# Performance work log

Hardware: AMD Instinct MI355X
Metric: run time of the kernel (lower is better)

## Reference

```python
import jax, jax.numpy as jnp
import numpy as np

N = 20000      # nodes (human PPI network scale)
E = 640000     # edges (avg degree 32)
PE, GOS, PROT = 128, 128, 480
OM_DIMS = [3, 3, 24, 24]          # transcriptome, proteome, effectome, interactome
D = 384                           # latent_space_dimension = 128 * 3 (jk 'cat')
H = 128                           # hidden_channels per layer
NEG_SLOPE = 0.1


def setup_inputs() -> dict:
    key = jax.random.key(0)
    ks = jax.random.split(key, 64)
    rn = lambda k, shp, s=0.05: jax.random.normal(k, shp, jnp.float32) * s
    inp = {
        "x": jax.random.normal(ks[0], (N, PE + GOS + PROT), jnp.float32),
        "x_ft": jax.random.normal(ks[1], (N, sum(OM_DIMS)), jnp.float32),
        "edge_index": jax.random.randint(ks[2], (2, E), 0, N),
    }
    i = 3
    def lin(fin, fout, name):
        nonlocal i
        inp["W_" + name] = rn(ks[i], (fin, fout)); inp["b_" + name] = jnp.zeros((fout,), jnp.float32)
        i += 1
    lin(PE, D, "pe"); lin(GOS, D, "gos"); lin(PROT, D, "prot")
    for j, d in enumerate(OM_DIMS):
        lin(d, D, f"om{j}")
    dims = [D, H, H, H]
    for j in range(3):
        lin(dims[j], dims[j + 1], f"c{j}")   # feature-branch GCN convs
        lin(dims[j], dims[j + 1], f"o{j}")   # omics-branch GCN convs
    lin(2 * D, D, "lat")
    lin(D, H, "drug"); lin(D, H, "dis")
    lin(H, 2, "odrug"); lin(H, 2, "odis")
    return inp


def _gcn(x, W, b, src, dst, deg_inv):
    # GCNConv(improved=True): A_hat = A + 2I, sym norm D^-1/2 A_hat D^-1/2
    h = x @ W                                  # [N, F_out]
    coef = deg_inv[src] * deg_inv[dst]         # [E]
    agg = jax.ops.segment_sum(h[src] * coef[:, None], dst, num_segments=N)
    agg = agg + h * (2.0 * deg_inv * deg_inv)[:, None]   # self loops (weight 2)
    return agg + b


def reference(x, x_ft, edge_index,
              W_pe, b_pe, W_gos, b_gos, W_prot, b_prot,
              W_om0, b_om0, W_om1, b_om1, W_om2, b_om2, W_om3, b_om3,
              W_c0, b_c0, W_o0, b_o0, W_c1, b_c1, W_o1, b_o1, W_c2, b_c2, W_o2, b_o2,
              W_lat, b_lat, W_drug, b_drug, W_dis, b_dis,
              W_odrug, b_odrug, W_odis, b_odis):
    act = lambda t: jax.nn.leaky_relu(t, NEG_SLOPE)
    src, dst = edge_index[0], edge_index[1]
    deg = jax.ops.segment_sum(jnp.ones((E,), jnp.float32), dst, num_segments=N) + 2.0
    deg_inv = jax.lax.rsqrt(deg)

    # encoders (features branch): pe | gosemsim | prot_emb slices of x
    pe = x[:, :PE]; gos = x[:, PE:PE + GOS]; prot = x[:, PE + GOS:PE + GOS + PROT]
    h = act(pe @ W_pe + b_pe + gos @ W_gos + b_gos + prot @ W_prot + b_prot)

    # encoders (omics branch): 3|3|24|24 slices of x_ft
    offs = np.cumsum([0] + OM_DIMS)
    Wom = [W_om0, W_om1, W_om2, W_om3]; bom = [b_om0, b_om1, b_om2, b_om3]
    g = act(sum(x_ft[:, offs[j]:offs[j + 1]] @ Wom[j] + bom[j] for j in range(4)))

    Wc = [W_c0, W_c1, W_c2]; bc = [b_c0, b_c1, b_c2]
    Wo = [W_o0, W_o1, W_o2]; bo = [b_o0, b_o1, b_o2]
    hs, gs = [], []
    for j in range(3):
        h = act(_gcn(h, Wc[j], bc[j], src, dst, deg_inv)); hs.append(h)
        g = act(_gcn(g, Wo[j], bo[j], src, dst, deg_inv)); gs.append(g)
    jk = jnp.concatenate(hs, axis=-1)          # [N, 384]
    jk_om = jnp.concatenate(gs, axis=-1)       # [N, 384]

    z = act(jnp.concatenate([jk, jk_om], axis=-1) @ W_lat + b_lat)  # [N, 384]
    drug = act(z @ W_drug + b_drug) @ W_odrug + b_odrug             # [N, 2]
    dis = act(z @ W_dis + b_dis) @ W_odis + b_odis                  # [N, 2]
    return jnp.concatenate([drug, dis], axis=-1)                    # [N, 4]
```

## Files before the change

kernel.cpp:

```cpp
#include <hip/hip_runtime.h>
#include <cstdint>

#define NN 20000
#define NNP 20096
#define NE 640000
#define NEG_SLOPE 0.1f
#define NSCAN 79
#define NSL 8
#define NPSL 2500
#define FBPS 160
#define NPART 8

typedef unsigned short ushort_t;
typedef __attribute__((ext_vector_type(8))) short short8;
typedef __attribute__((ext_vector_type(4))) float f32x4;
typedef __attribute__((ext_vector_type(2))) float f32x2;

__device__ __forceinline__ unsigned short f2bf(float f) {
    union { float f; unsigned u; } v; v.f = f;
    unsigned r = v.u + 0x7fffu + ((v.u >> 16) & 1u);
    return (unsigned short)(r >> 16);
}
__device__ __forceinline__ float bflo(unsigned u) { return __uint_as_float(u << 16); }
__device__ __forceinline__ float bfhi(unsigned u) { return __uint_as_float(u & 0xffff0000u); }

__device__ __forceinline__ int swz(int r) { return (r ^ (r >> 2)) & 3; }

__device__ __forceinline__ void gld_lds16(const void* g, void* l) {
    __builtin_amdgcn_global_load_lds(
        (const __attribute__((address_space(1))) void*)g,
        (__attribute__((address_space(3))) void*)l,
        16, 0, 0);
}

#define O_CAT   0
#define O_OM    282624
#define O_C0    307200
#define O_O0    356352
#define O_C1    405504
#define O_O1    421888
#define O_C2    438272
#define O_O2    454656
#define O_LAT   471040
#define O_HEADS 765952
#define WT_TOTAL 864256

__global__ __launch_bounds__(256) void pack_weights(
    const float* __restrict__ Wpe, const float* __restrict__ Wgos, const float* __restrict__ Wprot,
    const float* __restrict__ bpe, const float* __restrict__ bgos, const float* __restrict__ bprot,
    const float* __restrict__ Wom0, const float* __restrict__ Wom1,
    const float* __restrict__ Wom2, const float* __restrict__ Wom3,
    const float* __restrict__ bom0, const float* __restrict__ bom1,
    const float* __restrict__ bom2, const float* __restrict__ bom3,
    const float* __restrict__ Wc0, const float* __restrict__ Wo0,
    const float* __restrict__ Wc1, const float* __restrict__ Wo1,
    const float* __restrict__ Wc2, const float* __restrict__ Wo2,
    const float* __restrict__ Wlat,
    const float* __restrict__ Wdrug, const float* __restrict__ Wdis,
    const float* __restrict__ bdrug, const float* __restrict__ bdis,
    ushort_t* __restrict__ Wt, float* __restrict__ bcat, float* __restrict__ bomc,
    float* __restrict__ bheads, int* __restrict__ cnt8)
{
    int i = blockIdx.x * blockDim.x + threadIdx.x;
    if (i < 282624) {
        int m = i / 736, k = i % 736;
        float v = (k < 128) ? Wpe[k * 384 + m]
                : (k < 256) ? Wgos[(k - 128) * 384 + m]
                            : Wprot[(k - 256) * 384 + m];
        Wt[O_CAT + i] = f2bf(v);
        return;
    }
    i -= 282624;
    if (i < 24576) {
        int m = i / 64, k = i % 64;
        float v = (k < 3)  ? Wom0[k * 384 + m]
                : (k < 6)  ? Wom1[(k - 3) * 384 + m]
                : (k < 30) ? Wom2[(k - 6) * 384 + m]
                : (k < 54) ? Wom3[(k - 30) * 384 + m] : 0.f;
        Wt[O_OM + i] = f2bf(v);
        return;
    }
    i -= 24576;
    if (i < 49152) { int m = i / 384, k = i % 384; Wt[O_C0 + i] = f2bf(Wc0[k * 128 + m]); return; }
    i -= 49152;
    if (i < 49152) { int m = i / 384, k = i % 384; Wt[O_O0 + i] = f2bf(Wo0[k * 128 + m]); return; }
    i -= 49152;
    if (i < 16384) { int m = i / 128, k = i % 128; Wt[O_C1 + i] = f2bf(Wc1[k * 128 + m]); return; }
    i -= 16384;
    if (i < 16384) { int m = i / 128, k = i % 128; Wt[O_O1 + i] = f2bf(Wo1[k * 128 + m]); return; }
    i -= 16384;
    if (i < 16384) { int m = i / 128, k = i % 128; Wt[O_C2 + i] = f2bf(Wc2[k * 128 + m]); return; }
    i -= 16384;
    if (i < 16384) { int m = i / 128, k = i % 128; Wt[O_O2 + i] = f2bf(Wo2[k * 128 + m]); return; }
    i -= 16384;
    if (i < 294912) { int m = i / 768, k = i % 768; Wt[O_LAT + i] = f2bf(Wlat[k * 384 + m]); return; }
    i -= 294912;
    if (i < 98304) {
        int m = i / 384, k = i % 384;
        float v = (m < 128) ? Wdrug[k * 128 + m] : Wdis[k * 128 + (m - 128)];
        Wt[O_HEADS + i] = f2bf(v);
        return;
    }
    i -= 98304;
    if (i < 384) { bcat[i] = bpe[i] + bgos[i] + bprot[i]; return; }
    i -= 384;
    if (i < 384) { bomc[i] = bom0[i] + bom1[i] + bom2[i] + bom3[i]; return; }
    i -= 384;
    if (i < 256) { bheads[i] = (i < 128) ? bdrug[i] : bdis[i - 128]; return; }
    i -= 256;
    if (i < NN * NPART) { cnt8[i] = 0; return; }
}
#define PACK_TOTAL (WT_TOTAL + 384 + 384 + 256 + NN * NPART)

#define CVT_T1 (NN * 736 / 4)
__global__ __launch_bounds__(256) void convert_inputs(
    const float* __restrict__ x, const float* __restrict__ xft,
    ushort_t* __restrict__ xb, ushort_t* __restrict__ xftb)
{
    int i = blockIdx.x * blockDim.x + threadIdx.x;
    if (i < CVT_T1) {
        int base = i * 4;
        float4 v = *reinterpret_cast<const float4*>(&x[base]);
        unsigned long long p = (unsigned long long)f2bf(v.x)
                             | ((unsigned long long)f2bf(v.y) << 16)
                             | ((unsigned long long)f2bf(v.z) << 32)
                             | ((unsigned long long)f2bf(v.w) << 48);
        *reinterpret_cast<unsigned long long*>(&xb[base]) = p;
        return;
    }
    i -= CVT_T1;
    if (i < NN * 64) {
        int r = i >> 6, c = i & 63;
        float v = (c < 54) ? xft[r * 54 + c] : 0.f;
        xftb[i] = f2bf(v);
    }
}

__global__ __launch_bounds__(256) void count_deg_sliced(
    const int* __restrict__ src, const int* __restrict__ dst, int* __restrict__ cnt8)
{
    const int slice = blockIdx.x & (NSL - 1);
    const int blk = blockIdx.x >> 3;
    const int lo = slice * NPSL, hi = lo + NPSL;
    for (int e = blk * 256 + threadIdx.x; e < NE; e += FBPS * 256) {
        int d = dst[e];
        if (d >= lo && d < hi) {
            int p = (unsigned)src[e] / 2500u;
            atomicAdd(&cnt8[d * NPART + p], 1);
        }
    }
}

__global__ __launch_bounds__(256) void scan_blocksums(const int* __restrict__ cnt8, int* __restrict__ bsum,
                                                      float* __restrict__ deg_inv)
{
    __shared__ int s[256];
    int t = threadIdx.x, i = blockIdx.x * 256 + t;
    int v = 0;
    if (i < NN) {
        uint4 a = *reinterpret_cast<const uint4*>(&cnt8[i * NPART]);
        uint4 b = *reinterpret_cast<const uint4*>(&cnt8[i * NPART + 4]);
        v = (int)(a.x + a.y + a.z + a.w + b.x + b.y + b.z + b.w);
        deg_inv[i] = rsqrtf((float)v + 2.0f);
    }
    s[t] = v;
    __syncthreads();
    for (int off = 128; off; off >>= 1) {
        if (t < off) s[t] += s[t + off];
        __syncthreads();
    }
    if (t == 0) bsum[blockIdx.x] = s[0];
}

__global__ __launch_bounds__(128) void scan_tops(const int* __restrict__ bsum,
                                                 int* __restrict__ boff, int* __restrict__ ofsN)
{
    __shared__ int s[NSCAN];
    int t = threadIdx.x;
    if (t < NSCAN) s[t] = bsum[t];
    __syncthreads();
    if (t == 0) {
        int run = 0;
        for (int b = 0; b < NSCAN; b++) { int x = s[b]; s[b] = run; run += x; }
        ofsN[NN] = run;
    }
    __syncthreads();
    if (t < NSCAN) boff[t] = s[t];
}

__global__ __launch_bounds__(256) void scan_apply(const int* __restrict__ cnt8, const int* __restrict__ boff,
                                                  int* __restrict__ ofsN, int* __restrict__ cursor8)
{
    __shared__ int s[256];
    int t = threadIdx.x, i = blockIdx.x * 256 + t;
    int c[NPART];
    int v = 0;
    if (i < NN) {
        uint4 a = *reinterpret_cast<const uint4*>(&cnt8[i * NPART]);
        uint4 b = *reinterpret_cast<const uint4*>(&cnt8[i * NPART + 4]);
        c[0] = a.x; c[1] = a.y; c[2] = a.z; c[3] = a.w;
        c[4] = b.x; c[5] = b.y; c[6] = b.z; c[7] = b.w;
#pragma unroll
        for (int p = 0; p < NPART; p++) v += c[p];
    }
    s[t] = v;
    __syncthreads();
    for (int off = 1; off < 256; off <<= 1) {
        int u = (t >= off) ? s[t - off] : 0;
        __syncthreads();
        s[t] += u;
        __syncthreads();
    }
    if (i < NN) {
        int run = s[t] - v + boff[blockIdx.x];
        ofsN[i] = run;
#pragma unroll
        for (int p = 0; p < NPART; p++) { cursor8[i * NPART + p] = run; run += c[p]; }
    }
}

__global__ __launch_bounds__(256) void fill_csr_sliced(
    const int* __restrict__ src, const int* __restrict__ dst,
    const float* __restrict__ deg_inv, int* __restrict__ cursor8,
    uint2* __restrict__ csr_pk)
{
    const int slice = blockIdx.x & (NSL - 1);
    const int blk = blockIdx.x >> 3;
    const int lo = slice * NPSL, hi = lo + NPSL;
    for (int e = blk * 256 + threadIdx.x; e < NE; e += FBPS * 256) {
        int d = dst[e];
        if (d >= lo && d < hi) {
            int s = src[e];
            int pp = (unsigned)s / 2500u;
            int p = atomicAdd(&cursor8[d * NPART + pp], 1);
            float cf = deg_inv[s] * deg_inv[d];
            csr_pk[p] = make_uint2((unsigned)s * 512u, __float_as_uint(cf));
        }
    }
}

template<int BN, bool BIASACT, bool OUT_BF16>
__device__ __forceinline__ void gemm_body(
    ushort_t* As, ushort_t* Bs,
    const ushort_t* __restrict__ A, int lda,
    const ushort_t* __restrict__ Wt,
    const float* __restrict__ bias,
    float* __restrict__ Cf, ushort_t* __restrict__ Cb, int ldc,
    int nrows, int K, int row0, int col0)
{
    constexpr int BK = 32;
    constexpr int NI = (BN == 128) ? 4 : 2;

    const int t = threadIdx.x;
    const int w = t >> 6, lane = t & 63;
    const int wr = w >> 1, wc = w & 1;
    const int m16 = lane & 15, quad = lane >> 4;
    const int sr = lane >> 2;
    const int pgrp = lane & 3;

    f32x4 acc[4][NI];
#pragma unroll
    for (int mi = 0; mi < 4; mi++)
#pragma unroll
        for (int ni = 0; ni < NI; ni++) acc[mi][ni] = (f32x4)0.f;

    for (int k0 = 0; k0 < K; k0 += BK) {
#pragma unroll
        for (int p = 0; p < 2; p++) {
            int c = p * 4 + w;
            int r = c * 16 + sr;
            int q = pgrp ^ swz(r);
            gld_lds16(&A[(size_t)(row0 + r) * lda + k0 + q * 8], &As[c * 512]);
        }
#pragma unroll
        for (int p = 0; p < BN / 64; p++) {
            int c = p * 4 + w;
            int r = c * 16 + sr;
            int q = pgrp ^ swz(r);
            gld_lds16(&Wt[(size_t)(col0 + r) * K + k0 + q * 8], &Bs[c * 512]);
        }
        __syncthreads();

        short8 af[4], bfr[NI];
#pragma unroll
        for (int mi = 0; mi < 4; mi++) {
            int r = wr * 64 + mi * 16 + m16;
            int p = quad ^ swz(r);
            af[mi] = *reinterpret_cast<const short8*>(&As[r * 32 + p * 8]);
        }
#pragma unroll
        for (int ni = 0; ni < NI; ni++) {
            int n = wc * (NI * 16) + ni * 16 + m16;
            int p = quad ^ swz(n);
            bfr[ni] = *reinterpret_cast<const short8*>(&Bs[n * 32 + p * 8]);
        }
#pragma unroll
        for (int mi = 0; mi < 4; mi++)
#pragma unroll
            for (int ni = 0; ni < NI; ni++)
                acc[mi][ni] = __builtin_amdgcn_mfma_f32_16x16x32_bf16(af[mi], bfr[ni], acc[mi][ni], 0, 0, 0);
        __syncthreads();
    }

#pragma unroll
    for (int mi = 0; mi < 4; mi++) {
#pragma unroll
        for (int reg = 0; reg < 4; reg++) {
            int grow = row0 + wr * 64 + mi * 16 + quad * 4 + reg;
            if (grow >= nrows) continue;
#pragma unroll
            for (int ni = 0; ni < NI; ni++) {
                int gcol = col0 + wc * (NI * 16) + ni * 16 + m16;
                float v = acc[mi][ni][reg];
                if constexpr (BIASACT) {
                    v += bias[gcol];
                    v = (v > 0.f) ? v : NEG_SLOPE * v;
                }
                if constexpr (OUT_BF16) Cb[(size_t)grow * ldc + gcol] = f2bf(v);
                else                    Cf[(size_t)grow * ldc + gcol] = v;
            }
        }
    }
}

template<int BN, bool BIASACT, bool OUT_BF16>
__global__ __launch_bounds__(256) void mfma_gemm(
    const ushort_t* __restrict__ A, int lda,
    const ushort_t* __restrict__ Wt,
    const float* __restrict__ bias,
    float* __restrict__ Cf, ushort_t* __restrict__ Cb, int ldc,
    int nrows, int K)
{
    __shared__ ushort_t As[128 * 32];
    __shared__ ushort_t Bs[BN * 32];
    gemm_body<BN, BIASACT, OUT_BF16>(As, Bs, A, lda, Wt, bias, Cf, Cb, ldc, nrows, K,
                                     blockIdx.y * 128, blockIdx.x * BN);
}

__global__ __launch_bounds__(256) void mfma_gemm_dual(
    const ushort_t* __restrict__ A0, const ushort_t* __restrict__ A1, int lda,
    const ushort_t* __restrict__ W0, const ushort_t* __restrict__ W1,
    ushort_t* __restrict__ tmpI,
    int nrows, int K)
{
    __shared__ ushort_t As[128 * 32];
    __shared__ ushort_t Bs[64 * 32];
    const ushort_t* A  = blockIdx.z ? A1 : A0;
    const ushort_t* Wt = blockIdx.z ? W1 : W0;
    ushort_t*       Cb = tmpI + blockIdx.z * 128;
    gemm_body<64, false, true>(As, Bs, A, lda, Wt, nullptr, nullptr, Cb, 256, nrows, K,
                               blockIdx.y * 128, blockIdx.x * 64);
}

__global__ __launch_bounds__(256) void aggregate_fused(
    const ushort_t* __restrict__ tabI,
    const float* __restrict__ bc, const float* __restrict__ bo,
    const int* __restrict__ ofsN, const uint2* __restrict__ csr_pk,
    const float* __restrict__ deg_inv,
    ushort_t* __restrict__ outb, int hcol, int gcol)
{
    const int w = threadIdx.x >> 6, lane = threadIdx.x & 63;
    const int i = blockIdx.x * 4 + w;
    const int el = lane >> 5;
    const int fq = lane & 31;
    const int chain = fq >> 4;
    const unsigned lbyte = (unsigned)(fq * 16);
    const char* __restrict__ tb = (const char*)tabI;

    const int start = ofsN[i], end = ofsN[i + 1];
    const float di = deg_inv[i];
    const uint4 pv = *reinterpret_cast<const uint4*>(tb + ((unsigned)i * 512u + lbyte));

    float acc[8];
#pragma unroll
    for (int q = 0; q < 8; q++) acc[q] = 0.f;

#define FMA8(P, C) \
    acc[0] = fmaf(bflo(P.x), C, acc[0]); acc[1] = fmaf(bfhi(P.x), C, acc[1]); \
    acc[2] = fmaf(bflo(P.y), C, acc[2]); acc[3] = fmaf(bfhi(P.y), C, acc[3]); \
    acc[4] = fmaf(bflo(P.z), C, acc[4]); acc[5] = fmaf(bfhi(P.z), C, acc[5]); \
    acc[6] = fmaf(bflo(P.w), C, acc[6]); acc[7] = fmaf(bfhi(P.w), C, acc[7])

    int j = start + el;
    for (; j + 6 < end; j += 8) {
        uint2 e0 = csr_pk[j];
        uint2 e1 = csr_pk[j + 2];
        uint2 e2 = csr_pk[j + 4];
        uint2 e3 = csr_pk[j + 6];
        uint4 p0 = *reinterpret_cast<const uint4*>(tb + (e0.x + lbyte));
        uint4 p1 = *reinterpret_cast<const uint4*>(tb + (e1.x + lbyte));
        uint4 p2 = *reinterpret_cast<const uint4*>(tb + (e2.x + lbyte));
        uint4 p3 = *reinterpret_cast<const uint4*>(tb + (e3.x + lbyte));
        float c0 = __uint_as_float(e0.y), c1 = __uint_as_float(e1.y);
        float c2 = __uint_as_float(e2.y), c3 = __uint_as_float(e3.y);
        FMA8(p0, c0); FMA8(p1, c1); FMA8(p2, c2); FMA8(p3, c3);
    }
    for (; j < end; j += 2) {
        uint2 e0 = csr_pk[j];
        uint4 p0 = *reinterpret_cast<const uint4*>(tb + (e0.x + lbyte));
        float c0 = __uint_as_float(e0.y);
        FMA8(p0, c0);
    }
#undef FMA8

#pragma unroll
    for (int q = 0; q < 8; q++) acc[q] += __shfl_xor(acc[q], 32);

    if (el == 0) {
        const float* __restrict__ bias = chain ? bo : bc;
        const int coloff = (fq & 15) * 8;
        const float c = 2.f * di * di;
        float sv[8] = {bflo(pv.x), bfhi(pv.x), bflo(pv.y), bfhi(pv.y),
                       bflo(pv.z), bfhi(pv.z), bflo(pv.w), bfhi(pv.w)};
        uint4 o;
        unsigned* op = &o.x;
#pragma unroll
        for (int q = 0; q < 8; q += 2) {
            float v0 = fmaf(sv[q],     c, acc[q])     + bias[coloff + q];
            float v1 = fmaf(sv[q + 1], c, acc[q + 1]) + bias[coloff + q + 1];
            v0 = (v0 > 0.f) ? v0 : NEG_SLOPE * v0;
            v1 = (v1 > 0.f) ? v1 : NEG_SLOPE * v1;
            op[q >> 1] = (unsigned)f2bf(v0) | ((unsigned)f2bf(v1) << 16);
        }
        const int col = (chain ? gcol : hcol) + coloff;
        *reinterpret_cast<uint4*>(&outb[(size_t)i * 768 + col]) = o;
    }
}

__global__ __launch_bounds__(256) void heads_kernel(
    const float* __restrict__ tmpH,
    const float* __restrict__ Wod, const float* __restrict__ bod,
    const float* __restrict__ Wos, const float* __restrict__ bos,
    float* __restrict__ out)
{
    int w = threadIdx.x >> 6, lane = threadIdx.x & 63;
    int i = blockIdx.x * 4 + w;
    if (i >= NN) return;
    float a0 = 0.f, a1 = 0.f, d0 = 0.f, d1 = 0.f;
#pragma unroll
    for (int p = 0; p < 2; p++) {
        int k = lane + p * 64;
        float vd = tmpH[(size_t)i * 256 + k];
        float vs = tmpH[(size_t)i * 256 + 128 + k];
        a0 = fmaf(vd, Wod[k * 2 + 0], a0);
        a1 = fmaf(vd, Wod[k * 2 + 1], a1);
        d0 = fmaf(vs, Wos[k * 2 + 0], d0);
        d1 = fmaf(vs, Wos[k * 2 + 1], d1);
    }
    for (int off = 32; off; off >>= 1) {
        a0 += __shfl_down(a0, off);
        a1 += __shfl_down(a1, off);
        d0 += __shfl_down(d0, off);
        d1 += __shfl_down(d1, off);
    }
    if (lane == 0) {
        out[(size_t)i * 4 + 0] = a0 + bod[0];
        out[(size_t)i * 4 + 1] = a1 + bod[1];
        out[(size_t)i * 4 + 2] = d0 + bos[0];
        out[(size_t)i * 4 + 3] = d1 + bos[1];
    }
}

extern "C" void kernel_launch(void* const* d_in, const int* in_sizes, int n_in,
                              void* d_out, int out_size, void* d_ws, size_t ws_size,
                              hipStream_t stream)
{
    const float* x      = (const float*)d_in[0];
    const float* x_ft   = (const float*)d_in[1];
    const int*   eidx   = (const int*)d_in[2];
    const float* W_pe   = (const float*)d_in[3];
    const float* b_pe   = (const float*)d_in[4];
    const float* W_gos  = (const float*)d_in[5];
    const float* b_gos  = (const float*)d_in[6];
    const float* W_prot = (const float*)d_in[7];
    const float* b_prot = (const float*)d_in[8];
    const float* W_om0  = (const float*)d_in[9];
    const float* b_om0  = (const float*)d_in[10];
    const float* W_om1  = (const float*)d_in[11];
    const float* b_om1  = (const float*)d_in[12];
    const float* W_om2  = (const float*)d_in[13];
    const float* b_om2  = (const float*)d_in[14];
    const float* W_om3  = (const float*)d_in[15];
    const float* b_om3  = (const float*)d_in[16];
    const float* W_c[3] = {(const float*)d_in[17], (const float*)d_in[21], (const float*)d_in[25]};
    const float* b_c[3] = {(const float*)d_in[18], (const float*)d_in[22], (const float*)d_in[26]};
    const float* W_o[3] = {(const float*)d_in[19], (const float*)d_in[23], (const float*)d_in[27]};
    const float* b_o[3] = {(const float*)d_in[20], (const float*)d_in[24], (const float*)d_in[28]};
    const float* W_lat  = (const float*)d_in[29];
    const float* b_lat  = (const float*)d_in[30];
    const float* W_drug = (const float*)d_in[31];
    const float* b_drug = (const float*)d_in[32];
    const float* W_dis  = (const float*)d_in[33];
    const float* b_dis  = (const float*)d_in[34];
    const float* W_odrug= (const float*)d_in[35];
    const float* b_odrug= (const float*)d_in[36];
    const float* W_odis = (const float*)d_in[37];
    const float* b_odis = (const float*)d_in[38];
    float* out = (float*)d_out;

    const int* e_src = eidx;
    const int* e_dst = eidx + NE;

    char* p = (char*)d_ws;
    auto alloc = [&](size_t bytes) -> void* {
        void* r = (void*)p;
        p += (bytes + 255) & ~(size_t)255;
        return r;
    };
    ushort_t* Wt    = (ushort_t*)alloc((size_t)WT_TOTAL * 2);
    float* bcat     = (float*)alloc(384 * 4);
    float* bomc     = (float*)alloc(384 * 4);
    float* bheads   = (float*)alloc(256 * 4);
    float* deg_inv  = (float*)alloc((size_t)NN * 4);
    int*   cnt8     = (int*)alloc((size_t)NN * NPART * 4);
    int*   cursor8  = (int*)alloc((size_t)NN * NPART * 4);
    int*   ofsN     = (int*)alloc((size_t)(NN + 1) * 4);
    int*   bsum     = (int*)alloc((size_t)NSCAN * 4);
    int*   boff     = (int*)alloc((size_t)NSCAN * 4);
    uint2* csr_pk   = (uint2*)alloc((size_t)NE * 8);
    ushort_t* xb    = (ushort_t*)alloc((size_t)NNP * 736 * 2);
    ushort_t* xftb  = (ushort_t*)alloc((size_t)NNP * 64 * 2);
    ushort_t* h0b   = (ushort_t*)alloc((size_t)NNP * 384 * 2);
    ushort_t* g0b   = (ushort_t*)alloc((size_t)NNP * 384 * 2);
    ushort_t* jkb   = (ushort_t*)alloc((size_t)NNP * 768 * 2);
    ushort_t* zb    = (ushort_t*)alloc((size_t)NNP * 384 * 2);
    ushort_t* tmpI  = (ushort_t*)alloc((size_t)NNP * 256 * 2);
    float* tmpH     = (float*)alloc((size_t)NNP * 256 * 4);
    (void)ws_size; (void)in_sizes; (void)n_in; (void)out_size;

    pack_weights<<<dim3((PACK_TOTAL + 255) / 256), dim3(256), 0, stream>>>(
        W_pe, W_gos, W_prot, b_pe, b_gos, b_prot,
        W_om0, W_om1, W_om2, W_om3, b_om0, b_om1, b_om2, b_om3,
        W_c[0], W_o[0], W_c[1], W_o[1], W_c[2], W_o[2],
        W_lat, W_drug, W_dis, b_drug, b_dis, Wt, bcat, bomc, bheads, cnt8);

    convert_inputs<<<dim3((CVT_T1 + NN * 64 + 255) / 256), dim3(256), 0, stream>>>(x, x_ft, xb, xftb);

    count_deg_sliced<<<dim3(NSL * FBPS), dim3(256), 0, stream>>>(e_src, e_dst, cnt8);
    scan_blocksums<<<dim3(NSCAN), dim3(256), 0, stream>>>(cnt8, bsum, deg_inv);
    scan_tops<<<dim3(1), dim3(128), 0, stream>>>(bsum, boff, ofsN);
    scan_apply<<<dim3(NSCAN), dim3(256), 0, stream>>>(cnt8, boff, ofsN, cursor8);
    fill_csr_sliced<<<dim3(NSL * FBPS), dim3(256), 0, stream>>>(e_src, e_dst, deg_inv, cursor8, csr_pk);

    mfma_gemm<128, true, true><<<dim3(3, 157), dim3(256), 0, stream>>>(
        xb, 736, Wt + O_CAT, bcat, nullptr, h0b, 384, NN, 736);
    mfma_gemm<128, true, true><<<dim3(3, 157), dim3(256), 0, stream>>>(
        xftb, 64, Wt + O_OM, bomc, nullptr, g0b, 384, NN, 64);

    mfma_gemm_dual<<<dim3(2, 157, 2), dim3(256), 0, stream>>>(
        h0b, g0b, 384, Wt + O_C0, Wt + O_O0, tmpI, NN, 384);
    aggregate_fused<<<dim3(NN / 4), dim3(256), 0, stream>>>(
        tmpI, b_c[0], b_o[0], ofsN, csr_pk, deg_inv, jkb, 0, 384);

    mfma_gemm_dual<<<dim3(2, 157, 2), dim3(256), 0, stream>>>(
        jkb + 0, jkb + 384, 768, Wt + O_C1, Wt + O_O1, tmpI, NN, 128);
    aggregate_fused<<<dim3(NN / 4), dim3(256), 0, stream>>>(
        tmpI, b_c[1], b_o[1], ofsN, csr_pk, deg_inv, jkb, 128, 512);

    mfma_gemm_dual<<<dim3(2, 157, 2), dim3(256), 0, stream>>>(
        jkb + 128, jkb + 512, 768, Wt + O_C2, Wt + O_O2, tmpI, NN, 128);
    aggregate_fused<<<dim3(NN / 4), dim3(256), 0, stream>>>(
        tmpI, b_c[2], b_o[2], ofsN, csr_pk, deg_inv, jkb, 256, 640);

    mfma_gemm<128, true, true><<<dim3(3, 157), dim3(256), 0, stream>>>(
        jkb, 768, Wt + O_LAT, b_lat, nullptr, zb, 384, NN, 768);

    mfma_gemm<128, true, false><<<dim3(2, 157), dim3(256), 0, stream>>>(
        zb, 384, Wt + O_HEADS, bheads, tmpH, nullptr, 256, NN, 384);
    heads_kernel<<<dim3((NN + 3) / 4), dim3(256), 0, stream>>>(
        tmpH, W_odrug, b_odrug, W_odis, b_odis, out);
}
```

Baseline: 480.1 us.

## Merge prologue kernels, fuse scan tops, merge encoder GEMMs, fuse output heads

Weight packing, input conversion and degree counting now run in one launch, with cnt8 zeroed by a memset. The single-block scan_tops kernel is folded into scan_apply, where every block redundantly computes the block offsets. The two encoder GEMMs share one launch via blockIdx.z. The heads GEMM now applies bias, leaky-relu and the 2-wide output projection in its epilogue, so the fp32 intermediate tmpH and heads_kernel are gone. The aim is fewer launches and less global traffic, at the cost of more complex epilogues and the degree counting sharing a launch with conversion work.

```diff
diff --git a/kernel.cpp b/kernel.cpp
--- a/kernel.cpp
+++ b/kernel.cpp
@@ -14,7 +14,6 @@
 typedef unsigned short ushort_t;
 typedef __attribute__((ext_vector_type(8))) short short8;
 typedef __attribute__((ext_vector_type(4))) float f32x4;
-typedef __attribute__((ext_vector_type(2))) float f32x2;
 
 __device__ __forceinline__ unsigned short f2bf(float f) {
     union { float f; unsigned u; } v; v.f = f;
@@ -45,7 +44,16 @@
 #define O_HEADS 765952
 #define WT_TOTAL 864256
 
-__global__ __launch_bounds__(256) void pack_weights(
+#define PACK_TOTAL (WT_TOTAL + 384 + 384 + 256)
+#define CVT_T1 (NN * 736 / 4)
+#define P1_CNTB (NSL * FBPS)
+#define P1_CVTB ((CVT_T1 + NN * 64 + 255) / 256)
+#define P1_PKB  (PACK_TOTAL / 256)
+
+__global__ __launch_bounds__(256) void phase1(
+    const int* __restrict__ esrc, const int* __restrict__ edst, int* __restrict__ cnt8,
+    const float* __restrict__ x, const float* __restrict__ xft,
+    ushort_t* __restrict__ xb, ushort_t* __restrict__ xftb,
     const float* __restrict__ Wpe, const float* __restrict__ Wgos, const float* __restrict__ Wprot,
     const float* __restrict__ bpe, const float* __restrict__ bgos, const float* __restrict__ bprot,
     const float* __restrict__ Wom0, const float* __restrict__ Wom1,
@@ -59,95 +67,91 @@
     const float* __restrict__ Wdrug, const float* __restrict__ Wdis,
     const float* __restrict__ bdrug, const float* __restrict__ bdis,
     ushort_t* __restrict__ Wt, float* __restrict__ bcat, float* __restrict__ bomc,
-    float* __restrict__ bheads, int* __restrict__ cnt8)
-{
-    int i = blockIdx.x * blockDim.x + threadIdx.x;
-    if (i < 282624) {
-        int m = i / 736, k = i % 736;
-        float v = (k < 128) ? Wpe[k * 384 + m]
-                : (k < 256) ? Wgos[(k - 128) * 384 + m]
-                            : Wprot[(k - 256) * 384 + m];
-        Wt[O_CAT + i] = f2bf(v);
+    float* __restrict__ bheads)
+{
+    int bx = blockIdx.x;
+    if (bx < P1_CNTB) {
+        const int slice = bx & (NSL - 1);
+        const int blk = bx >> 3;
+        const int lo = slice * NPSL, hi = lo + NPSL;
+        for (int e = blk * 256 + threadIdx.x; e < NE; e += FBPS * 256) {
+            int d = edst[e];
+            if (d >= lo && d < hi) {
+                int p = (unsigned)esrc[e] / 2500u;
+                atomicAdd(&cnt8[d * NPART + p], 1);
+            }
+        }
         return;
     }
-    i -= 282624;
-    if (i < 24576) {
-        int m = i / 64, k = i % 64;
-        float v = (k < 3)  ? Wom0[k * 384 + m]
-                : (k < 6)  ? Wom1[(k - 3) * 384 + m]
-                : (k < 30) ? Wom2[(k - 6) * 384 + m]
-                : (k < 54) ? Wom3[(k - 30) * 384 + m] : 0.f;
-        Wt[O_OM + i] = f2bf(v);
+    bx -= P1_CNTB;
+    if (bx < P1_CVTB) {
+        int i = bx * 256 + threadIdx.x;
+        if (i < CVT_T1) {
+            int base = i * 4;
+            float4 v = *reinterpret_cast<const float4*>(&x[base]);
+            unsigned long long p = (unsigned long long)f2bf(v.x)
+                                 | ((unsigned long long)f2bf(v.y) << 16)
+                                 | ((unsigned long long)f2bf(v.z) << 32)
+                                 | ((unsigned long long)f2bf(v.w) << 48);
+            *reinterpret_cast<unsigned long long*>(&xb[base]) = p;
+            return;
+        }
+        i -= CVT_T1;
+        if (i < NN * 64) {
+            int r = i >> 6, c = i & 63;
+            float v = (c < 54) ? xft[r * 54 + c] : 0.f;
+            xftb[i] = f2bf(v);
+        }
         return;
     }
-    i -= 24576;
-    if (i < 49152) { int m = i / 384, k = i % 384; Wt[O_C0 + i] = f2bf(Wc0[k * 128 + m]); return; }
-    i -= 49152;
-    if (i < 49152) { int m = i / 384, k = i % 384; Wt[O_O0 + i] = f2bf(Wo0[k * 128 + m]); return; }
-    i -= 49152;
-    if (i < 16384) { int m = i / 128, k = i % 128; Wt[O_C1 + i] = f2bf(Wc1[k * 128 + m]); return; }
-    i -= 16384;
-    if (i < 16384) { int m = i / 128, k = i % 128; Wt[O_O1 + i] = f2bf(Wo1[k * 128 + m]); return; }
-    i -= 16384;
-    if (i < 16384) { int m = i / 128, k = i % 128; Wt[O_C2 + i] = f2bf(Wc2[k * 128 + m]); return; }
-    i -= 16384;
-    if (i < 16384) { int m = i / 128, k = i % 128; Wt[O_O2 + i] = f2bf(Wo2[k * 128 + m]); return; }
-    i -= 16384;
-    if (i < 294912) { int m = i / 768, k = i % 768; Wt[O_LAT + i] = f2bf(Wlat[k * 384 + m]); return; }
-    i -= 294912;
-    if (i < 98304) {
-        int m = i / 384, k = i % 384;
-        float v = (m < 128) ? Wdrug[k * 128 + m] : Wdis[k * 128 + (m - 128)];
-        Wt[O_HEADS + i] = f2bf(v);
-        return;
-    }
-    i -= 98304;
-    if (i < 384) { bcat[i] = bpe[i] + bgos[i] + bprot[i]; return; }
-    i -= 384;
-    if (i < 384) { bomc[i] = bom0[i] + bom1[i] + bom2[i] + bom3[i]; return; }
-    i -= 384;
-    if (i < 256) { bheads[i] = (i < 128) ? bdrug[i] : bdis[i - 128]; return; }
-    i -= 256;
-    if (i < NN * NPART) { cnt8[i] = 0; return; }
-}
-#define PACK_TOTAL (WT_TOTAL + 384 + 384 + 256 + NN * NPART)
-
-#define CVT_T1 (NN * 736 / 4)
-__global__ __launch_bounds__(256) void convert_inputs(
-    const float* __restrict__ x, const float* __restrict__ xft,
-    ushort_t* __restrict__ xb, ushort_t* __restrict__ xftb)
-{
-    int i = blockIdx.x * blockDim.x + threadIdx.x;
-    if (i < CVT_T1) {
-        int base = i * 4;
-        float4 v = *reinterpret_cast<const float4*>(&x[base]);
-        unsigned long long p = (unsigned long long)f2bf(v.x)
-                             | ((unsigned long long)f2bf(v.y) << 16)
-                             | ((unsigned long long)f2bf(v.z) << 32)
-                             | ((unsigned long long)f2bf(v.w) << 48);
-        *reinterpret_cast<unsigned long long*>(&xb[base]) = p;
-        return;
-    }
-    i -= CVT_T1;
-    if (i < NN * 64) {
-        int r = i >> 6, c = i & 63;
-        float v = (c < 54) ? xft[r * 54 + c] : 0.f;
-        xftb[i] = f2bf(v);
-    }
-}
-
-__global__ __launch_bounds__(256) void count_deg_sliced(
-    const int* __restrict__ src, const int* __restrict__ dst, int* __restrict__ cnt8)
-{
-    const int slice = blockIdx.x & (NSL - 1);
-    const int blk = blockIdx.x >> 3;
-    const int lo = slice * NPSL, hi = lo + NPSL;
-    for (int e = blk * 256 + threadIdx.x; e < NE; e += FBPS * 256) {
-        int d = dst[e];
-        if (d >= lo && d < hi) {
-            int p = (unsigned)src[e] / 2500u;
-            atomicAdd(&cnt8[d * NPART + p], 1);
-        }
+    bx -= P1_CVTB;
+    {
+        int i = bx * 256 + threadIdx.x;
+        if (i < 282624) {
+            int m = i / 736, k = i % 736;
+            float v = (k < 128) ? Wpe[k * 384 + m]
+                    : (k < 256) ? Wgos[(k - 128) * 384 + m]
+                                : Wprot[(k - 256) * 384 + m];
+            Wt[O_CAT + i] = f2bf(v);
+            return;
+        }
+        i -= 282624;
+        if (i < 24576) {
+            int m = i / 64, k = i % 64;
+            float v = (k < 3)  ? Wom0[k * 384 + m]
+                    : (k < 6)  ? Wom1[(k - 3) * 384 + m]
+                    : (k < 30) ? Wom2[(k - 6) * 384 + m]
+                    : (k < 54) ? Wom3[(k - 30) * 384 + m] : 0.f;
+            Wt[O_OM + i] = f2bf(v);
+            return;
+        }
+        i -= 24576;
+        if (i < 49152) { int m = i / 384, k = i % 384; Wt[O_C0 + i] = f2bf(Wc0[k * 128 + m]); return; }
+        i -= 49152;
+        if (i < 49152) { int m = i / 384, k = i % 384; Wt[O_O0 + i] = f2bf(Wo0[k * 128 + m]); return; }
+        i -= 49152;
+        if (i < 16384) { int m = i / 128, k = i % 128; Wt[O_C1 + i] = f2bf(Wc1[k * 128 + m]); return; }
+        i -= 16384;
+        if (i < 16384) { int m = i / 128, k = i % 128; Wt[O_O1 + i] = f2bf(Wo1[k * 128 + m]); return; }
+        i -= 16384;
+        if (i < 16384) { int m = i / 128, k = i % 128; Wt[O_C2 + i] = f2bf(Wc2[k * 128 + m]); return; }
+        i -= 16384;
+        if (i < 16384) { int m = i / 128, k = i % 128; Wt[O_O2 + i] = f2bf(Wo2[k * 128 + m]); return; }
+        i -= 16384;
+        if (i < 294912) { int m = i / 768, k = i % 768; Wt[O_LAT + i] = f2bf(Wlat[k * 384 + m]); return; }
+        i -= 294912;
+        if (i < 98304) {
+            int m = i / 384, k = i % 384;
+            float v = (m < 128) ? Wdrug[k * 128 + m] : Wdis[k * 128 + (m - 128)];
+            Wt[O_HEADS + i] = f2bf(v);
+            return;
+        }
+        i -= 98304;
+        if (i < 384) { bcat[i] = bpe[i] + bgos[i] + bprot[i]; return; }
+        i -= 384;
+        if (i < 384) { bomc[i] = bom0[i] + bom1[i] + bom2[i] + bom3[i]; return; }
+        i -= 384;
+        if (i < 256) { bheads[i] = (i < 128) ? bdrug[i] : bdis[i - 128]; return; }
     }
 }
 
@@ -172,27 +176,22 @@
     if (t == 0) bsum[blockIdx.x] = s[0];
 }
 
-__global__ __launch_bounds__(128) void scan_tops(const int* __restrict__ bsum,
-                                                 int* __restrict__ boff, int* __restrict__ ofsN)
-{
-    __shared__ int s[NSCAN];
-    int t = threadIdx.x;
-    if (t < NSCAN) s[t] = bsum[t];
+__global__ __launch_bounds__(256) void scan_apply(const int* __restrict__ cnt8, const int* __restrict__ bsum,
+                                                  int* __restrict__ ofsN, int* __restrict__ cursor8)
+{
+    __shared__ int s[256];
+    __shared__ int sb[NSCAN];
+    int t = threadIdx.x, i = blockIdx.x * 256 + t;
+    if (t < NSCAN) sb[t] = bsum[t];
     __syncthreads();
     if (t == 0) {
         int run = 0;
-        for (int b = 0; b < NSCAN; b++) { int x = s[b]; s[b] = run; run += x; }
-        ofsN[NN] = run;
+        for (int b = 0; b < NSCAN; b++) { int x2 = sb[b]; sb[b] = run; run += x2; }
+        if (blockIdx.x == 0) ofsN[NN] = run;
     }
     __syncthreads();
-    if (t < NSCAN) boff[t] = s[t];
-}
-
-__global__ __launch_bounds__(256) void scan_apply(const int* __restrict__ cnt8, const int* __restrict__ boff,
-                                                  int* __restrict__ ofsN, int* __restrict__ cursor8)
-{
-    __shared__ int s[256];
-    int t = threadIdx.x, i = blockIdx.x * 256 + t;
+    const int boff = sb[blockIdx.x];
+
     int c[NPART];
     int v = 0;
     if (i < NN) {
@@ -212,7 +211,7 @@
         __syncthreads();
     }
     if (i < NN) {
-        int run = s[t] - v + boff[blockIdx.x];
+        int run = s[t] - v + boff;
         ofsN[i] = run;
 #pragma unroll
         for (int p = 0; p < NPART; p++) { cursor8[i * NPART + p] = run; run += c[p]; }
@@ -239,14 +238,12 @@
     }
 }
 
-template<int BN, bool BIASACT, bool OUT_BF16>
-__device__ __forceinline__ void gemm_body(
+template<int BN>
+__device__ __forceinline__ void gemm_core(
     ushort_t* As, ushort_t* Bs,
     const ushort_t* __restrict__ A, int lda,
-    const ushort_t* __restrict__ Wt,
-    const float* __restrict__ bias,
-    float* __restrict__ Cf, ushort_t* __restrict__ Cb, int ldc,
-    int nrows, int K, int row0, int col0)
+    const ushort_t* __restrict__ Wt, int K, int row0, int col0,
+    f32x4 (&acc)[4][(BN == 128) ? 4 : 2])
 {
     constexpr int BK = 32;
     constexpr int NI = (BN == 128) ? 4 : 2;
@@ -258,7 +255,6 @@
     const int sr = lane >> 2;
     const int pgrp = lane & 3;
 
-    f32x4 acc[4][NI];
 #pragma unroll
     for (int mi = 0; mi < 4; mi++)
 #pragma unroll
@@ -301,7 +297,20 @@
                 acc[mi][ni] = __builtin_amdgcn_mfma_f32_16x16x32_bf16(af[mi], bfr[ni], acc[mi][ni], 0, 0, 0);
         __syncthreads();
     }
-
+}
+
+template<int BN, bool BIASACT, bool OUT_BF16>
+__device__ __forceinline__ void gemm_store(
+    const f32x4 (&acc)[4][(BN == 128) ? 4 : 2],
+    const float* __restrict__ bias,
+    float* __restrict__ Cf, ushort_t* __restrict__ Cb, int ldc,
+    int nrows, int row0, int col0)
+{
+    constexpr int NI = (BN == 128) ? 4 : 2;
+    const int t = threadIdx.x;
+    const int w = t >> 6, lane = t & 63;
+    const int wr = w >> 1, wc = w & 1;
+    const int m16 = lane & 15, quad = lane >> 4;
 #pragma unroll
     for (int mi = 0; mi < 4; mi++) {
 #pragma unroll
@@ -333,8 +342,29 @@
 {
     __shared__ ushort_t As[128 * 32];
     __shared__ ushort_t Bs[BN * 32];
-    gemm_body<BN, BIASACT, OUT_BF16>(As, Bs, A, lda, Wt, bias, Cf, Cb, ldc, nrows, K,
-                                     blockIdx.y * 128, blockIdx.x * BN);
+    f32x4 acc[4][(BN == 128) ? 4 : 2];
+    gemm_core<BN>(As, Bs, A, lda, Wt, K, blockIdx.y * 128, blockIdx.x * BN, acc);
+    gemm_store<BN, BIASACT, OUT_BF16>(acc, bias, Cf, Cb, ldc, nrows,
+                                      blockIdx.y * 128, blockIdx.x * BN);
+}
+
+__global__ __launch_bounds__(256) void mfma_gemm_mlp(
+    const ushort_t* __restrict__ xb, const ushort_t* __restrict__ xftb,
+    const ushort_t* __restrict__ Wt,
+    const float* __restrict__ bcat, const float* __restrict__ bomc,
+    ushort_t* __restrict__ h0b, ushort_t* __restrict__ g0b)
+{
+    __shared__ ushort_t As[128 * 32];
+    __shared__ ushort_t Bs[128 * 32];
+    f32x4 acc[4][4];
+    const int row0 = blockIdx.y * 128, col0 = blockIdx.x * 128;
+    if (blockIdx.z == 0) {
+        gemm_core<128>(As, Bs, xb, 736, Wt + O_CAT, 736, row0, col0, acc);
+        gemm_store<128, true, true>(acc, bcat, nullptr, h0b, 384, NN, row0, col0);
+    } else {
+        gemm_core<128>(As, Bs, xftb, 64, Wt + O_OM, 64, row0, col0, acc);
+        gemm_store<128, true, true>(acc, bomc, nullptr, g0b, 384, NN, row0, col0);
+    }
 }
 
 __global__ __launch_bounds__(256) void mfma_gemm_dual(
@@ -348,8 +378,90 @@
     const ushort_t* A  = blockIdx.z ? A1 : A0;
     const ushort_t* Wt = blockIdx.z ? W1 : W0;
     ushort_t*       Cb = tmpI + blockIdx.z * 128;
-    gemm_body<64, false, true>(As, Bs, A, lda, Wt, nullptr, nullptr, Cb, 256, nrows, K,
-                               blockIdx.y * 128, blockIdx.x * 64);
+    f32x4 acc[4][2];
+    gemm_core<64>(As, Bs, A, lda, Wt, K, blockIdx.y * 128, blockIdx.x * 64, acc);
+    gemm_store<64, false, true>(acc, nullptr, nullptr, Cb, 256, nrows,
+                                blockIdx.y * 128, blockIdx.x * 64);
+}
+
+__global__ __launch_bounds__(256) void mfma_gemm_heads(
+    const ushort_t* __restrict__ zb, const ushort_t* __restrict__ Wt,
+    const float* __restrict__ bheads,
+    const float* __restrict__ Wod, const float* __restrict__ bod,
+    const float* __restrict__ Wos, const float* __restrict__ bos,
+    float* __restrict__ out)
+{
+    __shared__ ushort_t As[128 * 32];
+    __shared__ ushort_t Bs[128 * 32];
+    f32x4 acc[4][4];
+    const int row0 = blockIdx.y * 128, col0 = blockIdx.x * 128;
+    gemm_core<128>(As, Bs, zb, 384, Wt + O_HEADS, 384, row0, col0, acc);
+
+    const float* __restrict__ Wh = col0 ? Wos : Wod;
+    const float* __restrict__ bh = col0 ? bos : bod;
+    const int t = threadIdx.x;
+    const int w = t >> 6, lane = t & 63;
+    const int wr = w >> 1, wc = w & 1;
+    const int m16 = lane & 15, quad = lane >> 4;
+
+    float w0[4], w1[4];
+#pragma unroll
+    for (int ni = 0; ni < 4; ni++) {
+        int k = wc * 64 + ni * 16 + m16;
+        w0[ni] = Wh[k * 2 + 0];
+        w1[ni] = Wh[k * 2 + 1];
+    }
+    float p0[16], p1[16];
+#pragma unroll
+    for (int mi = 0; mi < 4; mi++) {
+#pragma unroll
+        for (int reg = 0; reg < 4; reg++) {
+            float s0 = 0.f, s1 = 0.f;
+#pragma unroll
+            for (int ni = 0; ni < 4; ni++) {
+                int gcol = col0 + wc * 64 + ni * 16 + m16;
+                float v = acc[mi][ni][reg] + bheads[gcol];
+                v = (v > 0.f) ? v : NEG_SLOPE * v;
+                s0 = fmaf(v, w0[ni], s0);
+                s1 = fmaf(v, w1[ni], s1);
+            }
+            p0[mi * 4 + reg] = s0;
+            p1[mi * 4 + reg] = s1;
+        }
+    }
+#pragma unroll
+    for (int m = 1; m <= 8; m <<= 1) {
+#pragma unroll
+        for (int idx = 0; idx < 16; idx++) {
+            p0[idx] += __shfl_xor(p0[idx], m);
+            p1[idx] += __shfl_xor(p1[idx], m);
+        }
+    }
+    float* red = reinterpret_cast<float*>(As);
+    if (m16 == 0) {
+#pragma unroll
+        for (int mi = 0; mi < 4; mi++)
+#pragma unroll
+            for (int reg = 0; reg < 4; reg++) {
+                int row = mi * 16 + quad * 4 + reg;
+                int base = (((wr * 2 + wc) * 64) + row) * 2;
+                red[base + 0] = p0[mi * 4 + reg];
+                red[base + 1] = p1[mi * 4 + reg];
+            }
+    }
+    __syncthreads();
+    if (t < 128) {
+        int wr2 = t >> 6, row = t & 63;
+        int grow = row0 + wr2 * 64 + row;
+        if (grow < NN) {
+            int b0 = ((wr2 * 2 + 0) * 64 + row) * 2;
+            int b1 = ((wr2 * 2 + 1) * 64 + row) * 2;
+            float o0 = red[b0 + 0] + red[b1 + 0] + bh[0];
+            float o1 = red[b0 + 1] + red[b1 + 1] + bh[1];
+            out[(size_t)grow * 4 + (col0 ? 2 : 0) + 0] = o0;
+            out[(size_t)grow * 4 + (col0 ? 2 : 0) + 1] = o1;
+        }
+    }
 }
 
 __global__ __launch_bounds__(256) void aggregate_fused(
@@ -424,40 +536,6 @@
         }
         const int col = (chain ? gcol : hcol) + coloff;
         *reinterpret_cast<uint4*>(&outb[(size_t)i * 768 + col]) = o;
-    }
-}
-
-__global__ __launch_bounds__(256) void heads_kernel(
-    const float* __restrict__ tmpH,
-    const float* __restrict__ Wod, const float* __restrict__ bod,
-    const float* __restrict__ Wos, const float* __restrict__ bos,
-    float* __restrict__ out)
-{
-    int w = threadIdx.x >> 6, lane = threadIdx.x & 63;
-    int i = blockIdx.x * 4 + w;
-    if (i >= NN) return;
-    float a0 = 0.f, a1 = 0.f, d0 = 0.f, d1 = 0.f;
-#pragma unroll
-    for (int p = 0; p < 2; p++) {
-        int k = lane + p * 64;
-        float vd = tmpH[(size_t)i * 256 + k];
-        float vs = tmpH[(size_t)i * 256 + 128 + k];
-        a0 = fmaf(vd, Wod[k * 2 + 0], a0);
-        a1 = fmaf(vd, Wod[k * 2 + 1], a1);
-        d0 = fmaf(vs, Wos[k * 2 + 0], d0);
-        d1 = fmaf(vs, Wos[k * 2 + 1], d1);
-    }
-    for (int off = 32; off; off >>= 1) {
-        a0 += __shfl_down(a0, off);
-        a1 += __shfl_down(a1, off);
-        d0 += __shfl_down(d0, off);
-        d1 += __shfl_down(d1, off);
-    }
-    if (lane == 0) {
-        out[(size_t)i * 4 + 0] = a0 + bod[0];
-        out[(size_t)i * 4 + 1] = a1 + bod[1];
-        out[(size_t)i * 4 + 2] = d0 + bos[0];
-        out[(size_t)i * 4 + 3] = d1 + bos[1];
     }
 }
 
@@ -516,7 +594,6 @@
     int*   cursor8  = (int*)alloc((size_t)NN * NPART * 4);
     int*   ofsN     = (int*)alloc((size_t)(NN + 1) * 4);
     int*   bsum     = (int*)alloc((size_t)NSCAN * 4);
-    int*   boff     = (int*)alloc((size_t)NSCAN * 4);
     uint2* csr_pk   = (uint2*)alloc((size_t)NE * 8);
     ushort_t* xb    = (ushort_t*)alloc((size_t)NNP * 736 * 2);
     ushort_t* xftb  = (ushort_t*)alloc((size_t)NNP * 64 * 2);
@@ -525,27 +602,23 @@
     ushort_t* jkb   = (ushort_t*)alloc((size_t)NNP * 768 * 2);
     ushort_t* zb    = (ushort_t*)alloc((size_t)NNP * 384 * 2);
     ushort_t* tmpI  = (ushort_t*)alloc((size_t)NNP * 256 * 2);
-    float* tmpH     = (float*)alloc((size_t)NNP * 256 * 4);
     (void)ws_size; (void)in_sizes; (void)n_in; (void)out_size;
 
-    pack_weights<<<dim3((PACK_TOTAL + 255) / 256), dim3(256), 0, stream>>>(
+    hipMemsetAsync(cnt8, 0, (size_t)NN * NPART * 4, stream);
+    phase1<<<dim3(P1_CNTB + P1_CVTB + P1_PKB), dim3(256), 0, stream>>>(
+        e_src, e_dst, cnt8,
+        x, x_ft, xb, xftb,
         W_pe, W_gos, W_prot, b_pe, b_gos, b_prot,
         W_om0, W_om1, W_om2, W_om3, b_om0, b_om1, b_om2, b_om3,
         W_c[0], W_o[0], W_c[1], W_o[1], W_c[2], W_o[2],
-        W_lat, W_drug, W_dis, b_drug, b_dis, Wt, bcat, bomc, bheads, cnt8);
-
-    convert_inputs<<<dim3((CVT_T1 + NN * 64 + 255) / 256), dim3(256), 0, stream>>>(x, x_ft, xb, xftb);
-
-    count_deg_sliced<<<dim3(NSL * FBPS), dim3(256), 0, stream>>>(e_src, e_dst, cnt8);
+        W_lat, W_drug, W_dis, b_drug, b_dis, Wt, bcat, bomc, bheads);
+
     scan_blocksums<<<dim3(NSCAN), dim3(256), 0, stream>>>(cnt8, bsum, deg_inv);
-    scan_tops<<<dim3(1), dim3(128), 0, stream>>>(bsum, boff, ofsN);
-    scan_apply<<<dim3(NSCAN), dim3(256), 0, stream>>>(cnt8, boff, ofsN, cursor8);
+    scan_apply<<<dim3(NSCAN), dim3(256), 0, stream>>>(cnt8, bsum, ofsN, cursor8);
     fill_csr_sliced<<<dim3(NSL * FBPS), dim3(256), 0, stream>>>(e_src, e_dst, deg_inv, cursor8, csr_pk);
 
-    mfma_gemm<128, true, true><<<dim3(3, 157), dim3(256), 0, stream>>>(
-        xb, 736, Wt + O_CAT, bcat, nullptr, h0b, 384, NN, 736);
-    mfma_gemm<128, true, true><<<dim3(3, 157), dim3(256), 0, stream>>>(
-        xftb, 64, Wt + O_OM, bomc, nullptr, g0b, 384, NN, 64);
+    mfma_gemm_mlp<<<dim3(3, 157, 2), dim3(256), 0, stream>>>(
+        xb, xftb, Wt, bcat, bomc, h0b, g0b);
 
     mfma_gemm_dual<<<dim3(2, 157, 2), dim3(256), 0, stream>>>(
         h0b, g0b, 384, Wt + O_C0, Wt + O_O0, tmpI, NN, 384);
@@ -565,8 +638,6 @@
     mfma_gemm<128, true, true><<<dim3(3, 157), dim3(256), 0, stream>>>(
         jkb, 768, Wt + O_LAT, b_lat, nullptr, zb, 384, NN, 768);
 
-    mfma_gemm<128, true, false><<<dim3(2, 157), dim3(256), 0, stream>>>(
-        zb, 384, Wt + O_HEADS, bheads, tmpH, nullptr, 256, NN, 384);
-    heads_kernel<<<dim3((NN + 3) / 4), dim3(256), 0, stream>>>(
-        tmpH, W_odrug, b_odrug, W_odis, b_odis, out);
-}
+    mfma_gemm_heads<<<dim3(2, 157), dim3(256), 0, stream>>>(
+        zb, Wt, bheads, W_odrug, b_odrug, W_odis, b_odis, out);
+}
```

Result: faster. 452.9 us (-5.7%).
